# Kernel tuning notes

Measured on AMD Instinct MI355X. Metric: run time of the kernel, lower is better.

Reference implementation:

```python
import jax, jax.numpy as jnp
import numpy as np

S, B, D, H, L = 1024, 2, 1024, 16, 4
HD = D // H            # 64
MLP = 4 * D            # 4096
EPS = 1e-5


def _ln(x, w, b):
    m = x.mean(-1, keepdims=True)
    v = ((x - m) ** 2).mean(-1, keepdims=True)
    return (x - m) * jax.lax.rsqrt(v + EPS) * w + b


def _rotate_half(x):
    h = x.shape[-1] // 2
    return jnp.concatenate([-x[..., h:], x[..., :h]], axis=-1)


def _rope(t, cos, sin):
    # t: (B, S, H, HD); cos/sin: (S, HD) broadcast to (1, S, 1, HD)
    return t * cos[None, :, None, :] + _rotate_half(t) * sin[None, :, None, :]


def setup_inputs() -> dict:
    key = jax.random.key(0)
    ks = iter(jax.random.split(key, 64))

    def p(shape, scale=0.02):
        return jax.random.normal(next(ks), shape, jnp.float32) * scale

    return {
        "x": jax.random.normal(next(ks), (S, B, D), jnp.float32),
        "rotary_pos_emb": jax.random.normal(next(ks), (S, HD // 2), jnp.float32),
        # stacked per-layer params (leading dim L) for lax.scan
        "ln1_w": jnp.ones((L, D), jnp.float32), "ln1_b": jnp.zeros((L, D), jnp.float32),
        "in_w": p((L, 3 * D, D)), "in_b": jnp.zeros((L, 3 * D), jnp.float32),
        "out_w": p((L, D, D)), "out_b": jnp.zeros((L, D), jnp.float32),
        "ln2_w": jnp.ones((L, D), jnp.float32), "ln2_b": jnp.zeros((L, D), jnp.float32),
        "fc_w": p((L, MLP, D)), "fc_b": jnp.zeros((L, MLP), jnp.float32),
        "cp_w": p((L, D, MLP)), "cp_b": jnp.zeros((L, D), jnp.float32),
        # attention pooling head (qkv_bias=False in CrossAttention)
        "pn_q_w": jnp.ones((D,), jnp.float32), "pn_q_b": jnp.zeros((D,), jnp.float32),
        "pn_k_w": jnp.ones((D,), jnp.float32), "pn_k_b": jnp.zeros((D,), jnp.float32),
        "pn_v_w": jnp.ones((D,), jnp.float32), "pn_v_b": jnp.zeros((D,), jnp.float32),
        "pq_w": p((D, D)), "pk_w": p((D, D)), "pv_w": p((D, D)),
        "pp_w": p((D, D)), "pp_b": jnp.zeros((D,), jnp.float32),
    }


def reference(x, rotary_pos_emb, ln1_w, ln1_b, in_w, in_b, out_w, out_b,
              ln2_w, ln2_b, fc_w, fc_b, cp_w, cp_b,
              pn_q_w, pn_q_b, pn_k_w, pn_k_b, pn_v_w, pn_v_b,
              pq_w, pk_w, pv_w, pp_w, pp_b):
    # freqs (S, HD/2) -> cos/sin tiled twice along last dim: (S, HD)
    cos = jnp.tile(jnp.cos(rotary_pos_emb), (1, 2))
    sin = jnp.tile(jnp.sin(rotary_pos_emb), (1, 2))
    scale = 1.0 / np.sqrt(HD).astype(np.float32)

    def layer(h, p):
        l1w, l1b, iw, ib, ow, ob, l2w, l2b, fw, fb, cw, cb = p
        a = _ln(h, l1w, l1b)
        qkv = jnp.einsum('sbd,ed->sbe', a, iw) + ib           # (S,B,3D)
        qkv = qkv.reshape(S, B, 3, H, HD)
        q = jnp.transpose(qkv[:, :, 0], (1, 0, 2, 3))          # (B,S,H,HD)
        k = jnp.transpose(qkv[:, :, 1], (1, 0, 2, 3))
        v = jnp.transpose(qkv[:, :, 2], (1, 0, 2, 3))
        q = _rope(q, cos, sin)
        k = _rope(k, cos, sin)
        q, k, v = (t.transpose(0, 2, 1, 3) for t in (q, k, v))  # (B,H,S,HD)
        attn = jax.nn.softmax(jnp.einsum('bhsd,bhtd->bhst', q, k) * scale, axis=-1)
        o = jnp.einsum('bhst,bhtd->bhsd', attn, v)
        o = o.transpose(2, 0, 1, 3).reshape(S, B, D)           # back to (S,B,D)
        h = h + jnp.einsum('sbd,ed->sbe', o, ow) + ob          # residual + out_proj
        m = _ln(h, l2w, l2b)
        m = jax.nn.gelu(jnp.einsum('sbd,ed->sbe', m, fw) + fb, approximate=False)
        h = h + jnp.einsum('sbe,de->sbd', m, cw) + cb          # residual + c_proj
        return h, None

    h, _ = jax.lax.scan(layer, x, (ln1_w, ln1_b, in_w, in_b, out_w, out_b,
                                   ln2_w, ln2_b, fc_w, fc_b, cp_w, cp_b))

    # AttentionPoolingBlock: mean-pooled single query, cross-attend over tokens
    t = h.transpose(1, 0, 2)                                   # (B,N,C)
    xq = _ln(t.mean(1, keepdims=True), pn_q_w, pn_q_b)         # (B,1,C)
    xk = _ln(t, pn_k_w, pn_k_b)
    xv = _ln(t, pn_v_w, pn_v_b)
    q = (xq @ pq_w.T).reshape(B, 1, H, HD).transpose(0, 2, 1, 3)   # (B,H,1,HD)
    k = (xk @ pk_w.T).reshape(B, S, H, HD).transpose(0, 2, 1, 3)
    v = (xv @ pv_w.T).reshape(B, S, H, HD).transpose(0, 2, 1, 3)
    a = jax.nn.softmax(jnp.einsum('bhqd,bhtd->bhqt', q, k) * scale, axis=-1)
    o = jnp.einsum('bhqt,bhtd->bhqd', a, v).transpose(0, 2, 1, 3).reshape(B, 1, D)
    return (o @ pp_w.T + pp_b)[:, 0]                           # (B, D)
```

## Files before the change

### kernel.cpp

```cpp
#include <hip/hip_runtime.h>
#include <math.h>

#define S_LEN  1024
#define BATCH  2
#define DMODEL 1024
#define NHEAD  16
#define HDIM   64
#define NLAYER 4
#define MLPD   4096
#define MROWS  (S_LEN*BATCH)

typedef __attribute__((ext_vector_type(8))) short bf16x8_t;
typedef __attribute__((ext_vector_type(4))) float f32x4_t;

__device__ __forceinline__ unsigned short f2bf(float f) {
  union { float f; unsigned u; } c; c.f = f;
  return (unsigned short)((c.u + 0x7FFFu + ((c.u >> 16) & 1u)) >> 16);
}
__device__ __forceinline__ float bf2f(unsigned short u) {
  union { unsigned u; float f; } c; c.u = ((unsigned)u) << 16; return c.f;
}

__device__ __forceinline__ void gl_lds16(const unsigned short* g, unsigned short* l) {
  __builtin_amdgcn_global_load_lds(
      (const __attribute__((address_space(1))) unsigned int*)(g),
      (__attribute__((address_space(3))) unsigned int*)(l), 16, 0, 0);
}

__global__ __launch_bounds__(256) void w2bf_kernel(const float* __restrict__ src,
    unsigned short* __restrict__ dst, int n) {
  const int i = (blockIdx.x * 256 + threadIdx.x) * 8;
  if (i >= n) return;
  float4 v0 = *(const float4*)(src + i);
  float4 v1 = *(const float4*)(src + i + 4);
  ushort4 u0, u1;
  u0.x = f2bf(v0.x); u0.y = f2bf(v0.y); u0.z = f2bf(v0.z); u0.w = f2bf(v0.w);
  u1.x = f2bf(v1.x); u1.y = f2bf(v1.y); u1.z = f2bf(v1.z); u1.w = f2bf(v1.w);
  *(ushort4*)(dst + i)     = u0;
  *(ushort4*)(dst + i + 4) = u1;
}

__global__ __launch_bounds__(256) void trig_kernel(const float* __restrict__ rot,
    float2* __restrict__ tab) {
  const int i = blockIdx.x * 256 + threadIdx.x;
  const float f = rot[i];
  tab[i] = make_float2(cosf(f), sinf(f));
}

template<bool BF16OUT>
__global__ __launch_bounds__(256) void ln_kernel(const float* __restrict__ x,
    const float* __restrict__ w, const float* __restrict__ b,
    void* __restrict__ out, float inscale) {
  const int row = blockIdx.x;
  const int tid = threadIdx.x;
  const float* xr = x + (size_t)row * DMODEL;
  float4 v = *(const float4*)(xr + tid * 4);
  v.x *= inscale; v.y *= inscale; v.z *= inscale; v.w *= inscale;
  float s1 = v.x + v.y + v.z + v.w;
  float s2 = v.x*v.x + v.y*v.y + v.z*v.z + v.w*v.w;
  #pragma unroll
  for (int off = 32; off; off >>= 1) {
    s1 += __shfl_xor(s1, off);
    s2 += __shfl_xor(s2, off);
  }
  __shared__ float as1[4], as2[4];
  if ((tid & 63) == 0) { as1[tid >> 6] = s1; as2[tid >> 6] = s2; }
  __syncthreads();
  s1 = as1[0] + as1[1] + as1[2] + as1[3];
  s2 = as2[0] + as2[1] + as2[2] + as2[3];
  const float mean = s1 * (1.0f / DMODEL);
  const float var  = s2 * (1.0f / DMODEL) - mean * mean;
  const float r = rsqrtf(var + 1e-5f);
  float4 wv = *(const float4*)(w + tid * 4);
  float4 bv = *(const float4*)(b + tid * 4);
  float o0 = (v.x - mean) * r * wv.x + bv.x;
  float o1 = (v.y - mean) * r * wv.y + bv.y;
  float o2 = (v.z - mean) * r * wv.z + bv.z;
  float o3 = (v.w - mean) * r * wv.w + bv.w;
  if (BF16OUT) {
    ushort4 u; u.x = f2bf(o0); u.y = f2bf(o1); u.z = f2bf(o2); u.w = f2bf(o3);
    *(ushort4*)((unsigned short*)out + (size_t)row * DMODEL + tid * 4) = u;
  } else {
    float4 ov; ov.x = o0; ov.y = o1; ov.z = o2; ov.w = o3;
    *(float4*)((float*)out + (size_t)row * DMODEL + tid * 4) = ov;
  }
}

template<int NS, bool ADDDEST, bool DOLN>
__global__ __launch_bounds__(256) void reduce_ln_kernel(
    const float* __restrict__ part, const float* __restrict__ bias,
    float* __restrict__ dest, const float* __restrict__ lnw,
    const float* __restrict__ lnb, unsigned short* __restrict__ lnout) {
  const int row = blockIdx.x;
  const int tid = threadIdx.x;
  const size_t off = (size_t)row * DMODEL + tid * 4;
  float4 v;
  if (ADDDEST) v = *(const float4*)(dest + off);
  else { v.x = 0.f; v.y = 0.f; v.z = 0.f; v.w = 0.f; }
  if (bias) {
    float4 b4 = *(const float4*)(bias + tid * 4);
    v.x += b4.x; v.y += b4.y; v.z += b4.z; v.w += b4.w;
  }
  #pragma unroll
  for (int z = 0; z < NS; ++z) {
    float4 p = *(const float4*)(part + (size_t)z * (MROWS * DMODEL) + off);
    v.x += p.x; v.y += p.y; v.z += p.z; v.w += p.w;
  }
  *(float4*)(dest + off) = v;
  if (DOLN) {
    float s1 = v.x + v.y + v.z + v.w;
    float s2 = v.x*v.x + v.y*v.y + v.z*v.z + v.w*v.w;
    #pragma unroll
    for (int o = 32; o; o >>= 1) {
      s1 += __shfl_xor(s1, o);
      s2 += __shfl_xor(s2, o);
    }
    __shared__ float as1[4], as2[4];
    if ((tid & 63) == 0) { as1[tid >> 6] = s1; as2[tid >> 6] = s2; }
    __syncthreads();
    s1 = as1[0] + as1[1] + as1[2] + as1[3];
    s2 = as2[0] + as2[1] + as2[2] + as2[3];
    const float mean = s1 * (1.0f / DMODEL);
    const float var  = s2 * (1.0f / DMODEL) - mean * mean;
    const float r = rsqrtf(var + 1e-5f);
    float4 wv = *(const float4*)(lnw + tid * 4);
    float4 bv = *(const float4*)(lnb + tid * 4);
    ushort4 u;
    u.x = f2bf((v.x - mean) * r * wv.x + bv.x);
    u.y = f2bf((v.y - mean) * r * wv.y + bv.y);
    u.z = f2bf((v.z - mean) * r * wv.z + bv.z);
    u.w = f2bf((v.w - mean) * r * wv.w + bv.w);
    *(ushort4*)(lnout + (size_t)row * DMODEL + tid * 4) = u;
  }
}

template<int SPLIT, bool GELU, bool PARTIAL, bool OUTBF16>
__global__ __launch_bounds__(256, 3) void gemm_mfma(
    const unsigned short* __restrict__ A, const unsigned short* __restrict__ W,
    const float* __restrict__ bias, void* __restrict__ Cout,
    int M, int N, int K) {
  constexpr int BK = 32;
  __shared__ __align__(16) unsigned short As[2][128 * BK];
  __shared__ __align__(16) unsigned short Bs[2][128 * BK];
  const int tid  = threadIdx.x;
  const int wid  = tid >> 6;
  const int lane = tid & 63;
  const int lrow = lane & 15;
  const int lq   = lane >> 4;

  const int NB = gridDim.x, MB = gridDim.y;
  const int f = blockIdx.y * NB + blockIdx.x;
  const int xcd = f & 7;
  const int idx = f >> 3;
  const int m0 = (idx % MB) * 128;
  const int n0 = (xcd + (idx / MB) * 8) * 128;

  const int wm = (wid >> 1) * 64;
  const int wn = (wid & 1) * 64;
  const int Kc = K / SPLIT;
  const int kbase = blockIdx.z * Kc;

  f32x4_t acc[4][4];
  #pragma unroll
  for (int i = 0; i < 4; ++i)
    #pragma unroll
    for (int j = 0; j < 4; ++j) acc[i][j] = (f32x4_t){0.f, 0.f, 0.f, 0.f};

  const int c1 = tid, c2 = tid + 256;
  const unsigned short* Ag1 = A + (size_t)(m0 + (c1 >> 2)) * K + kbase + (c1 & 3) * 8;
  const unsigned short* Ag2 = A + (size_t)(m0 + (c2 >> 2)) * K + kbase + (c2 & 3) * 8;
  const unsigned short* Wg1 = W + (size_t)(n0 + (c1 >> 2)) * K + kbase + (c1 & 3) * 8;
  const unsigned short* Wg2 = W + (size_t)(n0 + (c2 >> 2)) * K + kbase + (c2 & 3) * 8;
  const int l1 = c1 * 8, l2 = c2 * 8;

  gl_lds16(Ag1, &As[0][l1]);
  gl_lds16(Ag2, &As[0][l2]);
  gl_lds16(Wg1, &Bs[0][l1]);
  gl_lds16(Wg2, &Bs[0][l2]);
  __syncthreads();

  int cur = 0;
  for (int k0 = 0; k0 < Kc; k0 += BK) {
    if (k0 + BK < Kc) {
      gl_lds16(Ag1 + k0 + BK, &As[cur ^ 1][l1]);
      gl_lds16(Ag2 + k0 + BK, &As[cur ^ 1][l2]);
      gl_lds16(Wg1 + k0 + BK, &Bs[cur ^ 1][l1]);
      gl_lds16(Wg2 + k0 + BK, &Bs[cur ^ 1][l2]);
    }

    bf16x8_t af[4], bfr[4];
    #pragma unroll
    for (int i = 0; i < 4; ++i)
      af[i] = *(const bf16x8_t*)&As[cur][(wm + i * 16 + lrow) * BK + lq * 8];
    #pragma unroll
    for (int j = 0; j < 4; ++j)
      bfr[j] = *(const bf16x8_t*)&Bs[cur][(wn + j * 16 + lrow) * BK + lq * 8];
    #pragma unroll
    for (int i = 0; i < 4; ++i)
      #pragma unroll
      for (int j = 0; j < 4; ++j)
        acc[i][j] = __builtin_amdgcn_mfma_f32_16x16x32_bf16(af[i], bfr[j], acc[i][j], 0, 0, 0);

    __syncthreads();
    cur ^= 1;
  }

  const size_t zoff = PARTIAL ? (size_t)blockIdx.z * ((size_t)M * N) : 0;
  float bj[4];
  #pragma unroll
  for (int j = 0; j < 4; ++j)
    bj[j] = (bias && (SPLIT == 1 || blockIdx.z == 0)) ? bias[n0 + wn + j * 16 + lrow] : 0.f;
  #pragma unroll
  for (int i = 0; i < 4; ++i) {
    #pragma unroll
    for (int r = 0; r < 4; ++r) {
      const int row = m0 + wm + i * 16 + lq * 4 + r;
      const size_t idx2 = (size_t)row * N + n0 + wn + lrow;
      #pragma unroll
      for (int j = 0; j < 4; ++j) {
        float val = acc[i][j][r] + bj[j];
        if (GELU)
          val = 0.5f * val * (1.0f + erff(val * 0.70710678118654752f));
        if (PARTIAL)
          ((float*)Cout)[zoff + idx2 + j * 16] = val;
        else if (OUTBF16)
          ((unsigned short*)Cout)[idx2 + j * 16] = f2bf(val);
        else
          ((float*)Cout)[idx2 + j * 16] = val;
      }
    }
  }
}

__global__ __launch_bounds__(256) void rope_kernel(const unsigned short* __restrict__ qkv,
    const float2* __restrict__ trig, unsigned short* __restrict__ qt,
    unsigned short* __restrict__ kt, unsigned short* __restrict__ vt) {
  const int idx = blockIdx.x * 256 + threadIdx.x;
  const int d  = idx & 63;
  const int hh = (idx >> 6) & 15;
  const int m  = idx >> 10;
  const int s  = m >> 1;
  const int b  = m & 1;
  const float2 t = trig[s * 32 + (d & 31)];
  const float cs = t.x;
  const float sn = t.y;
  const float sign = (d < 32) ? -1.0f : 1.0f;
  const size_t base  = (size_t)m * 3072 + hh * 64;
  const int bh = b * 16 + hh;
  const size_t obase = (((size_t)bh * 1024 + s) << 6) + d;
  float qv = bf2f(qkv[base + d]);
  float qp = bf2f(qkv[base + (d ^ 32)]);
  qt[obase] = f2bf(qv * cs + sign * qp * sn);
  float kv = bf2f(qkv[base + 1024 + d]);
  float kp = bf2f(qkv[base + 1024 + (d ^ 32)]);
  kt[obase] = f2bf(kv * cs + sign * kp * sn);
  vt[(((size_t)bh * 64 + d) << 10) + s] = qkv[base + 2048 + d];
}

__global__ __launch_bounds__(256, 3) void attn_kernel(
    const unsigned short* __restrict__ q, const unsigned short* __restrict__ k,
    const unsigned short* __restrict__ vtr, unsigned short* __restrict__ o) {
  const int tid  = threadIdx.x;
  const int wid  = tid >> 6;
  const int lane = tid & 63;
  const int col  = lane & 15;
  const int quad = lane >> 4;
  const int bh   = blockIdx.x >> 4;
  const int qw   = (blockIdx.x & 15) * 64 + wid * 16;

  __shared__ __align__(16) unsigned short Ks[64 * 72];
  __shared__ __align__(16) unsigned short Vs[64 * 72];
  __shared__ __align__(16) unsigned short Pl_[4][16 * 72];
  unsigned short* Pl = Pl_[wid];

  const unsigned short* kb = k   + ((size_t)bh << 16);
  const unsigned short* vb = vtr + ((size_t)bh << 16);

  bf16x8_t qa0, qa1;
  {
    const unsigned short* qp = q + ((((size_t)bh << 10) + qw + col) << 6) + quad * 8;
    qa0 = *(const bf16x8_t*)(qp);
    qa1 = *(const bf16x8_t*)(qp + 32);
  }

  f32x4_t oacc[4];
  #pragma unroll
  for (int j = 0; j < 4; ++j) oacc[j] = (f32x4_t){0.f, 0.f, 0.f, 0.f};
  float mr[4] = {-3.0e38f, -3.0e38f, -3.0e38f, -3.0e38f};
  float lr[4] = {0.f, 0.f, 0.f, 0.f};

  const int srow = tid >> 2;
  const int scol = (tid & 3) * 16;
  const unsigned short* gk0 = kb + (size_t)srow * 64 + scol;
  const unsigned short* gv0 = vb + (size_t)srow * 1024 + scol;
  unsigned short* lk0 = &Ks[srow * 72 + scol];
  unsigned short* lv0 = &Vs[srow * 72 + scol];

  {
    uint4 ka = *(const uint4*)(gk0);
    uint4 kc = *(const uint4*)(gk0 + 8);
    uint4 va = *(const uint4*)(gv0);
    uint4 vc = *(const uint4*)(gv0 + 8);
    *(uint4*)(lk0)     = ka;
    *(uint4*)(lk0 + 8) = kc;
    *(uint4*)(lv0)     = va;
    *(uint4*)(lv0 + 8) = vc;
  }
  __syncthreads();

  for (int t0 = 0; t0 < 1024; t0 += 64) {
    const bool more = (t0 + 64) < 1024;
    uint4 nka, nkc, nva, nvc;
    if (more) {
      const unsigned short* gk = gk0 + (size_t)(t0 + 64) * 64;
      const unsigned short* gv = gv0 + (t0 + 64);
      nka = *(const uint4*)(gk);
      nkc = *(const uint4*)(gk + 8);
      nva = *(const uint4*)(gv);
      nvc = *(const uint4*)(gv + 8);
    }

    f32x4_t sc[4];
    #pragma unroll
    for (int j = 0; j < 4; ++j) {
      bf16x8_t kf0 = *(const bf16x8_t*)&Ks[(j * 16 + col) * 72 + quad * 8];
      bf16x8_t kf1 = *(const bf16x8_t*)&Ks[(j * 16 + col) * 72 + quad * 8 + 32];
      f32x4_t c = (f32x4_t){0.f, 0.f, 0.f, 0.f};
      c = __builtin_amdgcn_mfma_f32_16x16x32_bf16(qa0, kf0, c, 0, 0, 0);
      c = __builtin_amdgcn_mfma_f32_16x16x32_bf16(qa1, kf1, c, 0, 0, 0);
      sc[j] = c;
    }

    #pragma unroll
    for (int r = 0; r < 4; ++r) {
      float s0 = sc[0][r] * 0.125f, s1 = sc[1][r] * 0.125f;
      float s2 = sc[2][r] * 0.125f, s3 = sc[3][r] * 0.125f;
      float rm = fmaxf(fmaxf(s0, s1), fmaxf(s2, s3));
      rm = fmaxf(rm, __shfl_xor(rm, 1));
      rm = fmaxf(rm, __shfl_xor(rm, 2));
      rm = fmaxf(rm, __shfl_xor(rm, 4));
      rm = fmaxf(rm, __shfl_xor(rm, 8));
      const float mn = fmaxf(mr[r], rm);
      const float alpha = __expf(mr[r] - mn);
      mr[r] = mn;
      const float p0 = __expf(s0 - mn), p1 = __expf(s1 - mn);
      const float p2 = __expf(s2 - mn), p3 = __expf(s3 - mn);
      float rs = p0 + p1 + p2 + p3;
      rs += __shfl_xor(rs, 1);
      rs += __shfl_xor(rs, 2);
      rs += __shfl_xor(rs, 4);
      rs += __shfl_xor(rs, 8);
      lr[r] = lr[r] * alpha + rs;
      #pragma unroll
      for (int j = 0; j < 4; ++j) oacc[j][r] *= alpha;
      const int prow = (quad * 4 + r) * 72;
      Pl[prow +  0 + col] = f2bf(p0);
      Pl[prow + 16 + col] = f2bf(p1);
      Pl[prow + 32 + col] = f2bf(p2);
      Pl[prow + 48 + col] = f2bf(p3);
    }

    bf16x8_t pa0 = *(const bf16x8_t*)&Pl[col * 72 + quad * 8];
    bf16x8_t pa1 = *(const bf16x8_t*)&Pl[col * 72 + quad * 8 + 32];
    #pragma unroll
    for (int j = 0; j < 4; ++j) {
      bf16x8_t vf0 = *(const bf16x8_t*)&Vs[(j * 16 + col) * 72 + quad * 8];
      bf16x8_t vf1 = *(const bf16x8_t*)&Vs[(j * 16 + col) * 72 + quad * 8 + 32];
      oacc[j] = __builtin_amdgcn_mfma_f32_16x16x32_bf16(pa0, vf0, oacc[j], 0, 0, 0);
      oacc[j] = __builtin_amdgcn_mfma_f32_16x16x32_bf16(pa1, vf1, oacc[j], 0, 0, 0);
    }

    __syncthreads();
    if (more) {
      *(uint4*)(lk0)     = nka;
      *(uint4*)(lk0 + 8) = nkc;
      *(uint4*)(lv0)     = nva;
      *(uint4*)(lv0 + 8) = nvc;
    }
    __syncthreads();
  }

  const int b = bh >> 4, hh = bh & 15;
  #pragma unroll
  for (int r = 0; r < 4; ++r) {
    const float inv = 1.0f / lr[r];
    const int sq = qw + quad * 4 + r;
    unsigned short* orow = o + (((size_t)sq * 2 + b) << 10) + hh * 64;
    #pragma unroll
    for (int j = 0; j < 4; ++j)
      orow[j * 16 + col] = f2bf(oacc[j][r] * inv);
  }
}

__global__ __launch_bounds__(256) void mean_kernel(const float* __restrict__ h,
    float* __restrict__ tsum) {
  const int idx = blockIdx.x * 256 + threadIdx.x;
  const int bd = idx & 2047;
  const int sc = idx >> 11;
  const int b = bd >> 10, d = bd & 1023;
  float sm = 0.f;
  for (int s = sc * 128; s < sc * 128 + 128; ++s)
    sm += h[(((size_t)s * 2 + b) << 10) + d];
  atomicAdd(&tsum[bd], sm);
}

__global__ __launch_bounds__(256) void smallmv_kernel(const float* __restrict__ in,
    const float* __restrict__ W, const float* __restrict__ bias,
    float* __restrict__ out) {
  const int lane = threadIdx.x & 63;
  const int n = blockIdx.x * 4 + (threadIdx.x >> 6);
  const int b = blockIdx.y;
  const float* wr = W + (size_t)n * 1024;
  const float* xr = in + (size_t)b * 1024;
  float sm = 0.f;
  #pragma unroll
  for (int j = 0; j < 4; ++j) {
    float4 wv = *(const float4*)(wr + lane * 4 + j * 256);
    float4 xv = *(const float4*)(xr + lane * 4 + j * 256);
    sm += wv.x * xv.x + wv.y * xv.y + wv.z * xv.z + wv.w * xv.w;
  }
  #pragma unroll
  for (int off = 32; off; off >>= 1) sm += __shfl_xor(sm, off);
  if (lane == 0) out[(size_t)b * 1024 + n] = sm + (bias ? bias[n] : 0.f);
}

__global__ __launch_bounds__(256) void pool_attn_part(const float* __restrict__ q,
    const float* __restrict__ k, const float* __restrict__ v,
    float* __restrict__ part) {
  const int wid  = (blockIdx.x * 256 + threadIdx.x) >> 6;
  const int lane = threadIdx.x & 63;
  const int bh = wid >> 4, kblk = wid & 15;
  const int b = bh >> 4, hh = bh & 15;
  const float qd = q[(size_t)b * 1024 + hh * 64 + lane];
  float mx = -3.0e38f, l = 0.f, acc = 0.f;
  for (int t = kblk * 64; t < kblk * 64 + 64; ++t) {
    const size_t ro = (((size_t)t * 2 + b) << 10) + hh * 64 + lane;
    float p = qd * k[ro];
    p += __shfl_xor(p, 32); p += __shfl_xor(p, 16); p += __shfl_xor(p, 8);
    p += __shfl_xor(p, 4);  p += __shfl_xor(p, 2);  p += __shfl_xor(p, 1);
    const float sc = p * 0.125f;
    const float mn = fmaxf(mx, sc);
    const float alpha = __expf(mx - mn);
    const float w = __expf(sc - mn);
    acc = acc * alpha + w * v[ro];
    l   = l * alpha + w;
    mx  = mn;
  }
  float* pp = part + (size_t)wid * 68;
  if (lane == 0) { pp[0] = mx; pp[1] = l; }
  pp[4 + lane] = acc;
}

__global__ __launch_bounds__(256) void pool_attn_comb(const float* __restrict__ part,
    float* __restrict__ o) {
  const int wid  = (blockIdx.x * 256 + threadIdx.x) >> 6;
  const int lane = threadIdx.x & 63;
  const float* pb = part + (size_t)wid * 16 * 68;
  float M = -3.0e38f;
  #pragma unroll
  for (int w = 0; w < 16; ++w) M = fmaxf(M, pb[w * 68]);
  float L = 0.f, O = 0.f;
  #pragma unroll
  for (int w = 0; w < 16; ++w) {
    const float e = __expf(pb[w * 68] - M);
    L += e * pb[w * 68 + 1];
    O += e * pb[w * 68 + 4 + lane];
  }
  const int b = wid >> 4, hh = wid & 15;
  o[(size_t)b * 1024 + hh * 64 + lane] = O / L;
}

extern "C" void kernel_launch(void* const* d_in, const int* in_sizes, int n_in,
                              void* d_out, int out_size, void* d_ws, size_t ws_size,
                              hipStream_t stream) {
  (void)in_sizes; (void)n_in; (void)out_size; (void)ws_size;
  const float* x     = (const float*)d_in[0];
  const float* rot   = (const float*)d_in[1];
  const float* ln1_w = (const float*)d_in[2];
  const float* ln1_b = (const float*)d_in[3];
  const float* in_w  = (const float*)d_in[4];
  const float* in_b  = (const float*)d_in[5];
  const float* out_w = (const float*)d_in[6];
  const float* out_b = (const float*)d_in[7];
  const float* ln2_w = (const float*)d_in[8];
  const float* ln2_b = (const float*)d_in[9];
  const float* fc_w  = (const float*)d_in[10];
  const float* fc_b  = (const float*)d_in[11];
  const float* cp_w  = (const float*)d_in[12];
  const float* cp_b  = (const float*)d_in[13];
  const float* pn_q_w = (const float*)d_in[14];
  const float* pn_q_b = (const float*)d_in[15];
  const float* pn_k_w = (const float*)d_in[16];
  const float* pn_k_b = (const float*)d_in[17];
  const float* pn_v_w = (const float*)d_in[18];
  const float* pn_v_b = (const float*)d_in[19];
  const float* pq_w  = (const float*)d_in[20];
  const float* pk_w  = (const float*)d_in[21];
  const float* pv_w  = (const float*)d_in[22];
  const float* pp_w  = (const float*)d_in[23];
  const float* pp_b  = (const float*)d_in[24];

  float* ws = (float*)d_ws;
  const size_t M1 = 1u << 20;
  float* h  = ws;
  float* a  = ws + 2 * M1;
  float* r1 = ws + 4 * M1;
  float* qt = ws + 12 * M1;
  float* kt = ws + 14 * M1;
  float* vt = ws + 16 * M1;
  float* o  = ws + 18 * M1;
  float* trig = ws + 19 * M1;
  float* wbf = ws + 20 * M1;
  unsigned short* a_bf  = (unsigned short*)a;
  unsigned short* r1_bf = (unsigned short*)r1;
  unsigned short* o_bf  = (unsigned short*)o;
  unsigned short* qt_bf = (unsigned short*)qt;
  unsigned short* kt_bf = (unsigned short*)kt;
  unsigned short* vt_bf = (unsigned short*)vt;
  unsigned short* wb_qkv = (unsigned short*)wbf;
  unsigned short* wb_out = wb_qkv + 3145728;
  unsigned short* wb_fc  = wb_out + 1048576;
  unsigned short* wb_cp  = wb_fc  + 4194304;
  float* part_op = r1;
  float* part_cp = qt;
  float* part_pool = ws + 5 * M1;
  float* tsum  = qt;
  float* xq    = qt + 2048;
  float* qpool = qt + 4096;
  float* opool = qt + 6144;
  float* ppart = qt + 8192;

  hipMemcpyAsync(h, x, 2 * M1 * sizeof(float), hipMemcpyDeviceToDevice, stream);

  trig_kernel<<<128, 256, 0, stream>>>(rot, (float2*)trig);
  ln_kernel<true><<<MROWS, 256, 0, stream>>>(h, ln1_w, ln1_b, a_bf, 1.0f);

  for (int l = 0; l < NLAYER; ++l) {
    w2bf_kernel<<<3145728 / 2048, 256, 0, stream>>>(in_w + (size_t)l * 3145728, wb_qkv, 3145728);
    w2bf_kernel<<<1048576 / 2048, 256, 0, stream>>>(out_w + (size_t)l * 1048576, wb_out, 1048576);
    w2bf_kernel<<<4194304 / 2048, 256, 0, stream>>>(fc_w + (size_t)l * 4194304, wb_fc, 4194304);
    w2bf_kernel<<<4194304 / 2048, 256, 0, stream>>>(cp_w + (size_t)l * 4194304, wb_cp, 4194304);

    gemm_mfma<1, false, false, true><<<dim3(3072 / 128, MROWS / 128, 1), 256, 0, stream>>>(
        a_bf, wb_qkv, in_b + l * 3072, r1_bf, MROWS, 3072, 1024);
    rope_kernel<<<8192, 256, 0, stream>>>(r1_bf, (const float2*)trig, qt_bf, kt_bf, vt_bf);
    attn_kernel<<<512, 256, 0, stream>>>(qt_bf, kt_bf, vt_bf, o_bf);
    gemm_mfma<4, false, true, false><<<dim3(1024 / 128, MROWS / 128, 4), 256, 0, stream>>>(
        o_bf, wb_out, nullptr, part_op, MROWS, 1024, 1024);
    reduce_ln_kernel<4, true, true><<<MROWS, 256, 0, stream>>>(
        part_op, out_b + l * 1024, h, ln2_w + l * DMODEL, ln2_b + l * DMODEL, a_bf);
    gemm_mfma<1, true, false, true><<<dim3(4096 / 128, MROWS / 128, 1), 256, 0, stream>>>(
        a_bf, wb_fc, fc_b + l * 4096, r1_bf, MROWS, 4096, 1024);
    gemm_mfma<4, false, true, false><<<dim3(1024 / 128, MROWS / 128, 4), 256, 0, stream>>>(
        r1_bf, wb_cp, nullptr, part_cp, MROWS, 1024, 4096);
    if (l < NLAYER - 1)
      reduce_ln_kernel<4, true, true><<<MROWS, 256, 0, stream>>>(
          part_cp, cp_b + l * 1024, h,
          ln1_w + (l + 1) * DMODEL, ln1_b + (l + 1) * DMODEL, a_bf);
    else
      reduce_ln_kernel<4, true, false><<<MROWS, 256, 0, stream>>>(
          part_cp, cp_b + l * 1024, h, nullptr, nullptr, nullptr);
  }

  hipMemsetAsync(tsum, 0, 2048 * sizeof(float), stream);
  mean_kernel<<<64, 256, 0, stream>>>(h, tsum);
  ln_kernel<false><<<BATCH, 256, 0, stream>>>(tsum, pn_q_w, pn_q_b, xq, 1.0f / S_LEN);
  ln_kernel<true><<<MROWS, 256, 0, stream>>>(h, pn_k_w, pn_k_b, a_bf, 1.0f);
  ln_kernel<true><<<MROWS, 256, 0, stream>>>(h, pn_v_w, pn_v_b, r1_bf, 1.0f);
  smallmv_kernel<<<dim3(256, BATCH), 256, 0, stream>>>(xq, pq_w, nullptr, qpool);
  w2bf_kernel<<<1048576 / 2048, 256, 0, stream>>>(pk_w, wb_qkv, 1048576);
  w2bf_kernel<<<1048576 / 2048, 256, 0, stream>>>(pv_w, wb_out, 1048576);
  gemm_mfma<2, false, true, false><<<dim3(1024 / 128, MROWS / 128, 2), 256, 0, stream>>>(
      a_bf, wb_qkv, nullptr, part_pool, MROWS, 1024, 1024);
  reduce_ln_kernel<2, false, false><<<MROWS, 256, 0, stream>>>(
      part_pool, nullptr, kt, nullptr, nullptr, nullptr);
  gemm_mfma<2, false, true, false><<<dim3(1024 / 128, MROWS / 128, 2), 256, 0, stream>>>(
      r1_bf, wb_out, nullptr, part_pool, MROWS, 1024, 1024);
  reduce_ln_kernel<2, false, false><<<MROWS, 256, 0, stream>>>(
      part_pool, nullptr, vt, nullptr, nullptr, nullptr);
  pool_attn_part<<<128, 256, 0, stream>>>(qpool, kt, vt, ppart);
  pool_attn_comb<<<8, 256, 0, stream>>>(ppart, opool);
  smallmv_kernel<<<dim3(256, BATCH), 256, 0, stream>>>(opool, pp_w, pp_b, (float*)d_out);
}
```

Before: 1.100 ms.

## Triple-buffer GEMM LDS staging with explicit vmcnt waits

Moves the bf16 MFMA GEMM from a double-buffered to a triple-buffered LDS pipeline. Global-to-LDS loads are now issued two K-tiles ahead. Each step waits with s_waitcnt vmcnt(4), so only the oldest tile must have landed, and uses a single raw s_barrier, replacing the old __syncthreads at the end of the loop. The aim is to hide more global load latency behind MFMA work. The cost is 50% more LDS per block, which may limit occupancy, and it depends on exact vmcnt accounting of the load instructions.

```diff
diff --git a/kernel.cpp b/kernel.cpp
--- a/kernel.cpp
+++ b/kernel.cpp
@@ -140,8 +140,8 @@
     const float* __restrict__ bias, void* __restrict__ Cout,
     int M, int N, int K) {
   constexpr int BK = 32;
-  __shared__ __align__(16) unsigned short As[2][128 * BK];
-  __shared__ __align__(16) unsigned short Bs[2][128 * BK];
+  __shared__ __align__(16) unsigned short As[3][128 * BK];
+  __shared__ __align__(16) unsigned short Bs[3][128 * BK];
   const int tid  = threadIdx.x;
   const int wid  = tid >> 6;
   const int lane = tid & 63;
@@ -159,6 +159,7 @@
   const int wn = (wid & 1) * 64;
   const int Kc = K / SPLIT;
   const int kbase = blockIdx.z * Kc;
+  const int nt = Kc / BK;
 
   f32x4_t acc[4][4];
   #pragma unroll
@@ -173,37 +174,48 @@
   const unsigned short* Wg2 = W + (size_t)(n0 + (c2 >> 2)) * K + kbase + (c2 & 3) * 8;
   const int l1 = c1 * 8, l2 = c2 * 8;
 
-  gl_lds16(Ag1, &As[0][l1]);
-  gl_lds16(Ag2, &As[0][l2]);
-  gl_lds16(Wg1, &Bs[0][l1]);
-  gl_lds16(Wg2, &Bs[0][l2]);
-  __syncthreads();
-
-  int cur = 0;
-  for (int k0 = 0; k0 < Kc; k0 += BK) {
-    if (k0 + BK < Kc) {
-      gl_lds16(Ag1 + k0 + BK, &As[cur ^ 1][l1]);
-      gl_lds16(Ag2 + k0 + BK, &As[cur ^ 1][l2]);
-      gl_lds16(Wg1 + k0 + BK, &Bs[cur ^ 1][l1]);
-      gl_lds16(Wg2 + k0 + BK, &Bs[cur ^ 1][l2]);
-    }
-
+  auto stage = [&](int t, int b) {
+    const int ko = t * BK;
+    gl_lds16(Ag1 + ko, &As[b][l1]);
+    gl_lds16(Ag2 + ko, &As[b][l2]);
+    gl_lds16(Wg1 + ko, &Bs[b][l1]);
+    gl_lds16(Wg2 + ko, &Bs[b][l2]);
+  };
+  auto compute = [&](int b) {
     bf16x8_t af[4], bfr[4];
     #pragma unroll
     for (int i = 0; i < 4; ++i)
-      af[i] = *(const bf16x8_t*)&As[cur][(wm + i * 16 + lrow) * BK + lq * 8];
+      af[i] = *(const bf16x8_t*)&As[b][(wm + i * 16 + lrow) * BK + lq * 8];
     #pragma unroll
     for (int j = 0; j < 4; ++j)
-      bfr[j] = *(const bf16x8_t*)&Bs[cur][(wn + j * 16 + lrow) * BK + lq * 8];
+      bfr[j] = *(const bf16x8_t*)&Bs[b][(wn + j * 16 + lrow) * BK + lq * 8];
     #pragma unroll
     for (int i = 0; i < 4; ++i)
       #pragma unroll
       for (int j = 0; j < 4; ++j)
         acc[i][j] = __builtin_amdgcn_mfma_f32_16x16x32_bf16(af[i], bfr[j], acc[i][j], 0, 0, 0);
-
-    __syncthreads();
-    cur ^= 1;
-  }
+  };
+
+  stage(0, 0);
+  stage(1, 1);
+
+  int cr = 0;
+  int cs = 2;
+  for (int t = 0; t < nt - 1; ++t) {
+    asm volatile("s_waitcnt vmcnt(4)" ::: "memory");
+    __builtin_amdgcn_sched_barrier(0);
+    __builtin_amdgcn_s_barrier();
+    __builtin_amdgcn_sched_barrier(0);
+    if (t + 2 < nt) stage(t + 2, cs);
+    compute(cr);
+    cr = (cr == 2) ? 0 : cr + 1;
+    cs = (cs == 2) ? 0 : cs + 1;
+  }
+  asm volatile("s_waitcnt vmcnt(0)" ::: "memory");
+  __builtin_amdgcn_sched_barrier(0);
+  __builtin_amdgcn_s_barrier();
+  __builtin_amdgcn_sched_barrier(0);
+  compute(cr);
 
   const size_t zoff = PARTIAL ? (size_t)blockIdx.z * ((size_t)M * N) : 0;
   float bj[4];
```

New measurement: 1.085 ms. No clear change (-1.4%).
